# Kernel optimization log

Hardware: AMD Instinct MI355X
Metric: run time of the kernel (lower is better)

## Reference

```python
import jax, jax.numpy as jnp
import numpy as np

B, S, E, H, TB = 2, 2048, 768, 12, 128
D = E // H  # head_dim = 64


def setup_inputs() -> dict:
    key = jax.random.key(0)
    ks = jax.random.split(key, 16)
    def w(k, shape):
        return (jax.random.normal(k, shape, dtype=jnp.float32) * 0.02)
    return {
        "query": jax.random.normal(ks[0], (B, S, E), dtype=jnp.float32),
        "key": jax.random.normal(ks[1], (B, S, E), dtype=jnp.float32),
        "value": jax.random.normal(ks[2], (B, S, E), dtype=jnp.float32),
        "task_bias": jax.random.normal(ks[3], (B, TB), dtype=jnp.float32),
        "attention_mask": jnp.ones((B, S), dtype=jnp.int32),
        # torch.nn.Linear weights are [out, in]
        "Wq": w(ks[4], (E, E)), "bq": jnp.zeros((E,), jnp.float32),
        "Wk": w(ks[5], (E, E)), "bk": jnp.zeros((E,), jnp.float32),
        "Wv": w(ks[6], (E, E)), "bv": jnp.zeros((E,), jnp.float32),
        "Wtb": w(ks[7], (H, TB)), "btb": jnp.zeros((H,), jnp.float32),
        "Wo": w(ks[8], (E, E)), "bo": jnp.zeros((E,), jnp.float32),
    }


def reference(query, key, value, task_bias, attention_mask,
              Wq, bq, Wk, bk, Wv, bv, Wtb, btb, Wo, bo):
    b, s, e = query.shape
    h, d = H, e // H
    # projections (torch Linear: x @ W^T + b), then split heads -> [b, h, s, d]
    q = (query @ Wq.T + bq).reshape(b, s, h, d).transpose(0, 2, 1, 3)
    k = (key @ Wk.T + bk).reshape(b, s, h, d).transpose(0, 2, 1, 3)
    v = (value @ Wv.T + bv).reshape(b, s, h, d).transpose(0, 2, 1, 3)
    # per-head additive task bias: [b, h] -> [b, h, 1, 1]
    tb = (task_bias @ Wtb.T + btb)[:, :, None, None]
    scores = jnp.einsum("bhqd,bhkd->bhqk", q, k) * (1.0 / (d ** 0.5)) + tb
    # 2-D mask broadcasts over query positions: [b, 1, 1, s]
    scores = jnp.where(attention_mask[:, None, None, :] == 0, -jnp.inf, scores)
    attn = jax.nn.softmax(scores, axis=-1)  # dropout is identity in eval mode
    ctx = jnp.einsum("bhqk,bhkd->bhqd", attn, v)
    ctx = ctx.transpose(0, 2, 1, 3).reshape(b, s, e)
    out = ctx @ Wo.T + bo
    return out, attn
```

## Files before the change

kernel.cpp:

```cpp
#include <hip/hip_runtime.h>
#include <math.h>

#define B_  2
#define S_  2048
#define E_  768
#define H_  12
#define TB_ 128
#define D_  64

typedef __attribute__((ext_vector_type(4))) float f32x4;
typedef __attribute__((ext_vector_type(8))) short bf16x8;

__device__ inline unsigned short bf16_rne(float x) {
    unsigned u = __float_as_uint(x);
    unsigned r = u + 0x7FFFu + ((u >> 16) & 1u);
    return (unsigned short)(r >> 16);
}
__device__ inline void split1(float x, unsigned short& h, unsigned short& l) {
    h = bf16_rne(x);
    float hf = __uint_as_float((unsigned)h << 16);
    l = bf16_rne(x - hf);
}

__device__ inline int lds_off(int row, int sh) {
    int ch = sh >> 3;
    int in = sh & 7;
    return row * 64 + (((ch ^ (row & 7)) << 3) | in);
}

__global__ __launch_bounds__(256)
void split_kernel(const float* __restrict__ in, unsigned short* __restrict__ hi,
                  unsigned short* __restrict__ lo, int n4) {
    int i = blockIdx.x * blockDim.x + threadIdx.x;
    int stride = gridDim.x * blockDim.x;
    for (; i < n4; i += stride) {
        float4 v = *(const float4*)&in[(size_t)i * 4];
        ushort4 h, l;
        split1(v.x, h.x, l.x); split1(v.y, h.y, l.y);
        split1(v.z, h.z, l.z); split1(v.w, h.w, l.w);
        *(ushort4*)&hi[(size_t)i * 4] = h;
        *(ushort4*)&lo[(size_t)i * 4] = l;
    }
}

template<int WPRE, int EPI>
__global__ __launch_bounds__(256)
void gemm_mfma(const unsigned short* __restrict__ Ahi_g,
               const unsigned short* __restrict__ Alo_g,
               const unsigned short* __restrict__ Whi_g,
               const unsigned short* __restrict__ Wlo_g,
               const float* __restrict__ Wf_g,
               const float* __restrict__ bias,
               float* __restrict__ Cf,
               unsigned short* __restrict__ Chi, unsigned short* __restrict__ Clo,
               int M, int N, int K) {
    __shared__ unsigned short Ahi[128 * 64];
    __shared__ unsigned short Alo[128 * 64];
    __shared__ unsigned short Whi[128 * 64];
    __shared__ unsigned short Wlo[128 * 64];

    const int m0 = blockIdx.y * 128;
    const int n0 = blockIdx.x * 128;
    const int tid  = threadIdx.x;
    const int wv   = tid >> 6;
    const int lane = tid & 63;
    const int l15  = lane & 15;
    const int quad = lane >> 4;

    f32x4 acc[2][8] = {};

    for (int k0 = 0; k0 < K; k0 += 64) {
        #pragma unroll
        for (int it = 0; it < 4; ++it) {
            int idx = it * 256 + tid;
            int r = idx >> 3, c8 = idx & 7;
            int o = r * 64 + (((c8 ^ (r & 7)) << 3));
            size_t ga = (size_t)(m0 + r) * K + k0 + c8 * 8;
            *(bf16x8*)&Ahi[o] = *(const bf16x8*)&Ahi_g[ga];
            *(bf16x8*)&Alo[o] = *(const bf16x8*)&Alo_g[ga];
            if constexpr (WPRE) {
                size_t gw = (size_t)(n0 + r) * K + k0 + c8 * 8;
                *(bf16x8*)&Whi[o] = *(const bf16x8*)&Whi_g[gw];
                *(bf16x8*)&Wlo[o] = *(const bf16x8*)&Wlo_g[gw];
            }
        }
        if constexpr (!WPRE) {
            const int row = tid >> 4, c4 = tid & 15;
            #pragma unroll
            for (int ps = 0; ps < 8; ++ps) {
                int r = ps * 16 + row;
                float4 w = *(const float4*)&Wf_g[(size_t)(n0 + r) * K + k0 + c4 * 4];
                ushort4 wh, wl;
                split1(w.x, wh.x, wl.x); split1(w.y, wh.y, wl.y);
                split1(w.z, wh.z, wl.z); split1(w.w, wh.w, wl.w);
                int o = lds_off(r, c4 * 4);
                *(ushort4*)&Whi[o] = wh;  *(ushort4*)&Wlo[o] = wl;
            }
        }
        __syncthreads();

        #pragma unroll
        for (int kk = 0; kk < 64; kk += 32) {
            bf16x8 aHi[2], aLo[2];
            #pragma unroll
            for (int ti = 0; ti < 2; ++ti) {
                int ar = wv * 32 + ti * 16 + l15;
                int sh = kk + quad * 8;
                aHi[ti] = *(const bf16x8*)&Ahi[lds_off(ar, sh)];
                aLo[ti] = *(const bf16x8*)&Alo[lds_off(ar, sh)];
            }
            #pragma unroll
            for (int tj = 0; tj < 8; ++tj) {
                int br = tj * 16 + l15;
                int sh = kk + quad * 8;
                bf16x8 bHi = *(const bf16x8*)&Whi[lds_off(br, sh)];
                bf16x8 bLo = *(const bf16x8*)&Wlo[lds_off(br, sh)];
                #pragma unroll
                for (int ti = 0; ti < 2; ++ti) {
                    acc[ti][tj] = __builtin_amdgcn_mfma_f32_16x16x32_bf16(aHi[ti], bHi, acc[ti][tj], 0, 0, 0);
                    acc[ti][tj] = __builtin_amdgcn_mfma_f32_16x16x32_bf16(aHi[ti], bLo, acc[ti][tj], 0, 0, 0);
                    acc[ti][tj] = __builtin_amdgcn_mfma_f32_16x16x32_bf16(aLo[ti], bHi, acc[ti][tj], 0, 0, 0);
                }
            }
        }
        __syncthreads();
    }

    #pragma unroll
    for (int ti = 0; ti < 2; ++ti) {
        const int ib = m0 + wv * 32 + ti * 16 + quad * 4;
        #pragma unroll
        for (int tj = 0; tj < 8; ++tj) {
            int col = n0 + tj * 16 + l15;
            float bv = bias[col];
            f32x4 a = acc[ti][tj];
            #pragma unroll
            for (int r = 0; r < 4; ++r) {
                float val = a[r] + bv;
                if constexpr (EPI == 0) {
                    Cf[(size_t)(ib + r) * N + col] = val;
                } else if constexpr (EPI == 1) {
                    unsigned short hh, ll;
                    split1(val, hh, ll);
                    Chi[(size_t)(ib + r) * N + col] = hh;
                    Clo[(size_t)(ib + r) * N + col] = ll;
                } else {
                    int token = ib + r;
                    int bt = token >> 11, s = token & (S_ - 1);
                    int hh_ = col >> 6, d = col & 63;
                    size_t oa = ((size_t)(bt * H_ + hh_) * 64 + d) * S_ + s;
                    unsigned short hh, ll;
                    split1(val, hh, ll);
                    Chi[oa] = hh;
                    Clo[oa] = ll;
                }
            }
        }
    }
}

__global__ void tb_kernel(const float* __restrict__ task_bias,
                          const float* __restrict__ Wtb,
                          const float* __restrict__ btb,
                          float* __restrict__ tb) {
    int t = threadIdx.x;
    if (t < B_ * H_) {
        int b = t / H_, h = t % H_;
        float s = 0.f;
        for (int i = 0; i < TB_; ++i)
            s += task_bias[b * TB_ + i] * Wtb[h * TB_ + i];
        tb[t] = s + btb[h];
    }
}

__global__ __launch_bounds__(256)
void scores_kernel(const unsigned short* __restrict__ qhi_g,
                   const unsigned short* __restrict__ qlo_g,
                   const unsigned short* __restrict__ khi_g,
                   const unsigned short* __restrict__ klo_g,
                   const int* __restrict__ mask, const float* __restrict__ tb,
                   float* __restrict__ attn, float* __restrict__ rowsum) {
    __shared__ unsigned short Qhi[128 * 64];
    __shared__ unsigned short Qlo[128 * 64];
    __shared__ unsigned short Khi[128 * 64];
    __shared__ unsigned short Klo[128 * 64];

    const int bh = blockIdx.z;
    const int b = bh / H_, h = bh % H_;
    const int i0 = blockIdx.y * 128;
    const int j0 = blockIdx.x * 128;
    const int tid  = threadIdx.x;
    const int wv   = tid >> 6;
    const int lane = tid & 63;
    const int l15  = lane & 15;
    const int quad = lane >> 4;

    #pragma unroll
    for (int it = 0; it < 4; ++it) {
        int idx = it * 256 + tid;
        int r = idx >> 3, c8 = idx & 7;
        int o = r * 64 + (((c8 ^ (r & 7)) << 3));
        size_t gq = ((size_t)b * S_ + i0 + r) * E_ + h * D_ + c8 * 8;
        size_t gk = ((size_t)b * S_ + j0 + r) * E_ + h * D_ + c8 * 8;
        *(bf16x8*)&Qhi[o] = *(const bf16x8*)&qhi_g[gq];
        *(bf16x8*)&Qlo[o] = *(const bf16x8*)&qlo_g[gq];
        *(bf16x8*)&Khi[o] = *(const bf16x8*)&khi_g[gk];
        *(bf16x8*)&Klo[o] = *(const bf16x8*)&klo_g[gk];
    }
    __syncthreads();

    f32x4 acc[2][8] = {};
    #pragma unroll
    for (int kk = 0; kk < 64; kk += 32) {
        bf16x8 aHi[2], aLo[2];
        #pragma unroll
        for (int ti = 0; ti < 2; ++ti) {
            int ar = wv * 32 + ti * 16 + l15;
            int sh = kk + quad * 8;
            aHi[ti] = *(const bf16x8*)&Qhi[lds_off(ar, sh)];
            aLo[ti] = *(const bf16x8*)&Qlo[lds_off(ar, sh)];
        }
        #pragma unroll
        for (int tj = 0; tj < 8; ++tj) {
            int br = tj * 16 + l15;
            int sh = kk + quad * 8;
            bf16x8 bHi = *(const bf16x8*)&Khi[lds_off(br, sh)];
            bf16x8 bLo = *(const bf16x8*)&Klo[lds_off(br, sh)];
            #pragma unroll
            for (int ti = 0; ti < 2; ++ti) {
                acc[ti][tj] = __builtin_amdgcn_mfma_f32_16x16x32_bf16(aHi[ti], bHi, acc[ti][tj], 0, 0, 0);
                acc[ti][tj] = __builtin_amdgcn_mfma_f32_16x16x32_bf16(aHi[ti], bLo, acc[ti][tj], 0, 0, 0);
                acc[ti][tj] = __builtin_amdgcn_mfma_f32_16x16x32_bf16(aLo[ti], bHi, acc[ti][tj], 0, 0, 0);
            }
        }
    }

    const float tbv = tb[bh];
    const int* mrow = mask + b * S_ + j0;
    int m_[8];
    #pragma unroll
    for (int tj = 0; tj < 8; ++tj) m_[tj] = mrow[tj * 16 + l15];

    float* attnbase = attn + (size_t)bh * S_ * S_;
    #pragma unroll
    for (int ti = 0; ti < 2; ++ti) {
        float rs[4] = {0.f, 0.f, 0.f, 0.f};
        const int ib = i0 + wv * 32 + ti * 16 + quad * 4;
        #pragma unroll
        for (int tj = 0; tj < 8; ++tj) {
            f32x4 a = acc[ti][tj];
            #pragma unroll
            for (int r = 0; r < 4; ++r) {
                float sc = a[r] * 0.125f + tbv;
                float p = m_[tj] ? __expf(sc) : 0.f;
                attnbase[(size_t)(ib + r) * S_ + j0 + tj * 16 + l15] = p;
                rs[r] += p;
            }
        }
        #pragma unroll
        for (int off = 1; off < 16; off <<= 1) {
            #pragma unroll
            for (int r = 0; r < 4; ++r)
                rs[r] += __shfl_xor(rs[r], off, 64);
        }
        if (l15 == 0) {
            #pragma unroll
            for (int r = 0; r < 4; ++r)
                atomicAdd(&rowsum[(size_t)bh * S_ + ib + r], rs[r]);
        }
    }
}

__global__ __launch_bounds__(256)
void ctx_mfma(float* __restrict__ attn, const float* __restrict__ rowsum,
              const unsigned short* __restrict__ Vthi_g,
              const unsigned short* __restrict__ Vtlo_g,
              unsigned short* __restrict__ ctxhi, unsigned short* __restrict__ ctxlo) {
    __shared__ unsigned short Phi[64 * 64];
    __shared__ unsigned short Plo[64 * 64];
    __shared__ unsigned short Vhi[64 * 64];
    __shared__ unsigned short Vlo[64 * 64];
    __shared__ float invs[64];

    const int bh = blockIdx.y;
    const int b = bh / H_, h = bh % H_;
    const int i0 = blockIdx.x * 64;
    const int tid  = threadIdx.x;
    const int wv   = tid >> 6;
    const int lane = tid & 63;
    const int l15  = lane & 15;
    const int quad = lane >> 4;

    if (tid < 64)
        invs[tid] = 1.0f / rowsum[(size_t)bh * S_ + i0 + tid];
    __syncthreads();

    f32x4 acc[4] = {};

    for (int kc = 0; kc < S_; kc += 64) {
        #pragma unroll
        for (int it = 0; it < 4; ++it) {
            int idx = it * 256 + tid;
            int row = idx >> 4, c4 = idx & 15;
            size_t pa = ((size_t)bh * S_ + i0 + row) * S_ + kc + c4 * 4;
            float4 p = *(const float4*)&attn[pa];
            float iv = invs[row];
            p.x *= iv; p.y *= iv; p.z *= iv; p.w *= iv;
            *(float4*)&attn[pa] = p;
            ushort4 ph, pl;
            split1(p.x, ph.x, pl.x); split1(p.y, ph.y, pl.y);
            split1(p.z, ph.z, pl.z); split1(p.w, ph.w, pl.w);
            int o = lds_off(row, c4 * 4);
            *(ushort4*)&Phi[o] = ph;  *(ushort4*)&Plo[o] = pl;
        }
        #pragma unroll
        for (int it = 0; it < 2; ++it) {
            int idx = it * 256 + tid;
            int r = idx >> 3, c8 = idx & 7;
            int o = r * 64 + (((c8 ^ (r & 7)) << 3));
            size_t va = ((size_t)bh * 64 + r) * S_ + kc + c8 * 8;
            *(bf16x8*)&Vhi[o] = *(const bf16x8*)&Vthi_g[va];
            *(bf16x8*)&Vlo[o] = *(const bf16x8*)&Vtlo_g[va];
        }
        __syncthreads();

        #pragma unroll
        for (int kk = 0; kk < 64; kk += 32) {
            int sh = kk + quad * 8;
            bf16x8 aH = *(const bf16x8*)&Phi[lds_off(wv * 16 + l15, sh)];
            bf16x8 aL = *(const bf16x8*)&Plo[lds_off(wv * 16 + l15, sh)];
            #pragma unroll
            for (int tj = 0; tj < 4; ++tj) {
                bf16x8 bH = *(const bf16x8*)&Vhi[lds_off(tj * 16 + l15, sh)];
                bf16x8 bL = *(const bf16x8*)&Vlo[lds_off(tj * 16 + l15, sh)];
                acc[tj] = __builtin_amdgcn_mfma_f32_16x16x32_bf16(aH, bH, acc[tj], 0, 0, 0);
                acc[tj] = __builtin_amdgcn_mfma_f32_16x16x32_bf16(aH, bL, acc[tj], 0, 0, 0);
                acc[tj] = __builtin_amdgcn_mfma_f32_16x16x32_bf16(aL, bH, acc[tj], 0, 0, 0);
            }
        }
        __syncthreads();
    }

    const int ib = i0 + wv * 16 + quad * 4;
    #pragma unroll
    for (int tj = 0; tj < 4; ++tj) {
        int d = tj * 16 + l15;
        f32x4 a = acc[tj];
        #pragma unroll
        for (int r = 0; r < 4; ++r) {
            unsigned short hh, ll;
            split1(a[r], hh, ll);
            size_t oa = ((size_t)b * S_ + ib + r) * E_ + h * D_ + d;
            ctxhi[oa] = hh;
            ctxlo[oa] = ll;
        }
    }
}

extern "C" void kernel_launch(void* const* d_in, const int* in_sizes, int n_in,
                              void* d_out, int out_size, void* d_ws, size_t ws_size,
                              hipStream_t stream) {
    const float* query     = (const float*)d_in[0];
    const float* key       = (const float*)d_in[1];
    const float* value     = (const float*)d_in[2];
    const float* task_bias = (const float*)d_in[3];
    const int*   mask      = (const int*)  d_in[4];
    const float* Wq  = (const float*)d_in[5];
    const float* bq  = (const float*)d_in[6];
    const float* Wk  = (const float*)d_in[7];
    const float* bk  = (const float*)d_in[8];
    const float* Wv  = (const float*)d_in[9];
    const float* bv  = (const float*)d_in[10];
    const float* Wtb = (const float*)d_in[11];
    const float* btb = (const float*)d_in[12];
    const float* Wo  = (const float*)d_in[13];
    const float* bo  = (const float*)d_in[14];

    const size_t BSE = (size_t)B_ * S_ * E_;
    const size_t EE  = (size_t)E_ * E_;
    float* out  = (float*)d_out;
    float* attn = (float*)d_out + BSE;

    unsigned short* qhi  = (unsigned short*)d_ws;
    unsigned short* qlo  = qhi  + BSE;
    unsigned short* khi  = qlo  + BSE;
    unsigned short* klo  = khi  + BSE;
    unsigned short* vthi = klo  + BSE;
    unsigned short* vtlo = vthi + BSE;
    unsigned short* chi  = vtlo + BSE;
    unsigned short* clo  = chi  + BSE;
    float* rowsum = (float*)(clo + BSE);
    float* tbws   = rowsum + (size_t)B_ * H_ * S_;

    unsigned short* aqhi = (unsigned short*)attn;
    unsigned short* aqlo = aqhi + BSE;
    unsigned short* akhi = aqlo + BSE;
    unsigned short* aklo = akhi + BSE;
    unsigned short* avhi = aklo + BSE;
    unsigned short* avlo = avhi + BSE;
    unsigned short* wqhi = avlo + BSE;
    unsigned short* wqlo = wqhi + EE;
    unsigned short* wkhi = wqlo + EE;
    unsigned short* wklo = wkhi + EE;
    unsigned short* wvhi = wklo + EE;
    unsigned short* wvlo = wvhi + EE;

    hipMemsetAsync(rowsum, 0, (size_t)B_ * H_ * S_ * sizeof(float), stream);

    const dim3 blk(256);

    split_kernel<<<dim3(2048), blk, 0, stream>>>(query, aqhi, aqlo, (int)(BSE / 4));
    split_kernel<<<dim3(2048), blk, 0, stream>>>(key,   akhi, aklo, (int)(BSE / 4));
    split_kernel<<<dim3(2048), blk, 0, stream>>>(value, avhi, avlo, (int)(BSE / 4));
    split_kernel<<<dim3(576),  blk, 0, stream>>>(Wq, wqhi, wqlo, (int)(EE / 4));
    split_kernel<<<dim3(576),  blk, 0, stream>>>(Wk, wkhi, wklo, (int)(EE / 4));
    split_kernel<<<dim3(576),  blk, 0, stream>>>(Wv, wvhi, wvlo, (int)(EE / 4));
    tb_kernel<<<1, 64, 0, stream>>>(task_bias, Wtb, btb, tbws);

    const dim3 gProj(E_ / 128, (B_ * S_) / 128);
    gemm_mfma<1, 1><<<gProj, blk, 0, stream>>>(aqhi, aqlo, wqhi, wqlo, nullptr,
                                               bq, nullptr, qhi, qlo,
                                               B_ * S_, E_, E_);
    gemm_mfma<1, 1><<<gProj, blk, 0, stream>>>(akhi, aklo, wkhi, wklo, nullptr,
                                               bk, nullptr, khi, klo,
                                               B_ * S_, E_, E_);
    gemm_mfma<1, 2><<<gProj, blk, 0, stream>>>(avhi, avlo, wvhi, wvlo, nullptr,
                                               bv, nullptr, vthi, vtlo,
                                               B_ * S_, E_, E_);

    const dim3 gSc(S_ / 128, S_ / 128, B_ * H_);
    scores_kernel<<<gSc, blk, 0, stream>>>(qhi, qlo, khi, klo, mask, tbws, attn, rowsum);

    const dim3 gCtx(S_ / 64, B_ * H_);
    ctx_mfma<<<gCtx, blk, 0, stream>>>(attn, rowsum, vthi, vtlo, chi, clo);

    gemm_mfma<0, 0><<<gProj, blk, 0, stream>>>(chi, clo, nullptr, nullptr, Wo,
                                               bo, out, nullptr, nullptr,
                                               B_ * S_, E_, E_);
}
```

Measured before the change: 923.1 us.

## Fuse attention into flash-style kernel and recompute normalized probabilities separately

Replaces the scores-then-context pipeline with a fused kernel that computes unnormalized exp scores, feeds them through LDS into the PV MFMA, and tracks row sums, so the large attn matrix no longer has to be re-read and rewritten by the context kernel. A second kernel then recomputes QK^T and writes the normalized attn output using the stored inverse row sums, which drops the atomics and the memset. The three QKV projections are merged into one launch, and Wo is pre-split into bf16 hi/lo buffers so the output GEMM no longer splits it per tile. The cost is computing QK^T twice and skipping max-subtraction in softmax, which relies on the scores being small enough not to overflow exp.

Result: faster. 812.1 us (-12.0%).

```diff
diff --git a/kernel.cpp b/kernel.cpp
--- a/kernel.cpp
+++ b/kernel.cpp
@@ -43,21 +43,31 @@
     }
 }
 
-template<int WPRE, int EPI>
 __global__ __launch_bounds__(256)
-void gemm_mfma(const unsigned short* __restrict__ Ahi_g,
-               const unsigned short* __restrict__ Alo_g,
-               const unsigned short* __restrict__ Whi_g,
-               const unsigned short* __restrict__ Wlo_g,
-               const float* __restrict__ Wf_g,
-               const float* __restrict__ bias,
-               float* __restrict__ Cf,
-               unsigned short* __restrict__ Chi, unsigned short* __restrict__ Clo,
-               int M, int N, int K) {
-    __shared__ unsigned short Ahi[128 * 64];
-    __shared__ unsigned short Alo[128 * 64];
-    __shared__ unsigned short Whi[128 * 64];
-    __shared__ unsigned short Wlo[128 * 64];
+void qkv_gemm(const unsigned short* __restrict__ aqh, const unsigned short* __restrict__ aql,
+              const unsigned short* __restrict__ akh, const unsigned short* __restrict__ akl,
+              const unsigned short* __restrict__ avh, const unsigned short* __restrict__ avl,
+              const unsigned short* __restrict__ wqh, const unsigned short* __restrict__ wql,
+              const unsigned short* __restrict__ wkh, const unsigned short* __restrict__ wkl,
+              const unsigned short* __restrict__ wvh, const unsigned short* __restrict__ wvl,
+              const float* __restrict__ bq, const float* __restrict__ bk,
+              const float* __restrict__ bv,
+              unsigned short* __restrict__ qh, unsigned short* __restrict__ ql,
+              unsigned short* __restrict__ kh, unsigned short* __restrict__ kl,
+              unsigned short* __restrict__ vth, unsigned short* __restrict__ vtl) {
+    __shared__ unsigned short Ahs[128 * 64];
+    __shared__ unsigned short Als[128 * 64];
+    __shared__ unsigned short Whs[128 * 64];
+    __shared__ unsigned short Wls[128 * 64];
+
+    const int z = blockIdx.z;
+    const unsigned short* Ah_g = z == 0 ? aqh : (z == 1 ? akh : avh);
+    const unsigned short* Al_g = z == 0 ? aql : (z == 1 ? akl : avl);
+    const unsigned short* Wh_g = z == 0 ? wqh : (z == 1 ? wkh : wvh);
+    const unsigned short* Wl_g = z == 0 ? wql : (z == 1 ? wkl : wvl);
+    const float* bias = z == 0 ? bq : (z == 1 ? bk : bv);
+    unsigned short* Ch = z == 0 ? qh : (z == 1 ? kh : vth);
+    unsigned short* Cl = z == 0 ? ql : (z == 1 ? kl : vtl);
 
     const int m0 = blockIdx.y * 128;
     const int n0 = blockIdx.x * 128;
@@ -66,6 +76,7 @@
     const int lane = tid & 63;
     const int l15  = lane & 15;
     const int quad = lane >> 4;
+    const int K = E_, N = E_;
 
     f32x4 acc[2][8] = {};
 
@@ -76,26 +87,11 @@
             int r = idx >> 3, c8 = idx & 7;
             int o = r * 64 + (((c8 ^ (r & 7)) << 3));
             size_t ga = (size_t)(m0 + r) * K + k0 + c8 * 8;
-            *(bf16x8*)&Ahi[o] = *(const bf16x8*)&Ahi_g[ga];
-            *(bf16x8*)&Alo[o] = *(const bf16x8*)&Alo_g[ga];
-            if constexpr (WPRE) {
-                size_t gw = (size_t)(n0 + r) * K + k0 + c8 * 8;
-                *(bf16x8*)&Whi[o] = *(const bf16x8*)&Whi_g[gw];
-                *(bf16x8*)&Wlo[o] = *(const bf16x8*)&Wlo_g[gw];
-            }
-        }
-        if constexpr (!WPRE) {
-            const int row = tid >> 4, c4 = tid & 15;
-            #pragma unroll
-            for (int ps = 0; ps < 8; ++ps) {
-                int r = ps * 16 + row;
-                float4 w = *(const float4*)&Wf_g[(size_t)(n0 + r) * K + k0 + c4 * 4];
-                ushort4 wh, wl;
-                split1(w.x, wh.x, wl.x); split1(w.y, wh.y, wl.y);
-                split1(w.z, wh.z, wl.z); split1(w.w, wh.w, wl.w);
-                int o = lds_off(r, c4 * 4);
-                *(ushort4*)&Whi[o] = wh;  *(ushort4*)&Wlo[o] = wl;
-            }
+            *(bf16x8*)&Ahs[o] = *(const bf16x8*)&Ah_g[ga];
+            *(bf16x8*)&Als[o] = *(const bf16x8*)&Al_g[ga];
+            size_t gw = (size_t)(n0 + r) * K + k0 + c8 * 8;
+            *(bf16x8*)&Whs[o] = *(const bf16x8*)&Wh_g[gw];
+            *(bf16x8*)&Wls[o] = *(const bf16x8*)&Wl_g[gw];
         }
         __syncthreads();
 
@@ -106,15 +102,15 @@
             for (int ti = 0; ti < 2; ++ti) {
                 int ar = wv * 32 + ti * 16 + l15;
                 int sh = kk + quad * 8;
-                aHi[ti] = *(const bf16x8*)&Ahi[lds_off(ar, sh)];
-                aLo[ti] = *(const bf16x8*)&Alo[lds_off(ar, sh)];
+                aHi[ti] = *(const bf16x8*)&Ahs[lds_off(ar, sh)];
+                aLo[ti] = *(const bf16x8*)&Als[lds_off(ar, sh)];
             }
             #pragma unroll
             for (int tj = 0; tj < 8; ++tj) {
                 int br = tj * 16 + l15;
                 int sh = kk + quad * 8;
-                bf16x8 bHi = *(const bf16x8*)&Whi[lds_off(br, sh)];
-                bf16x8 bLo = *(const bf16x8*)&Wlo[lds_off(br, sh)];
+                bf16x8 bHi = *(const bf16x8*)&Whs[lds_off(br, sh)];
+                bf16x8 bLo = *(const bf16x8*)&Wls[lds_off(br, sh)];
                 #pragma unroll
                 for (int ti = 0; ti < 2; ++ti) {
                     acc[ti][tj] = __builtin_amdgcn_mfma_f32_16x16x32_bf16(aHi[ti], bHi, acc[ti][tj], 0, 0, 0);
@@ -132,27 +128,22 @@
         #pragma unroll
         for (int tj = 0; tj < 8; ++tj) {
             int col = n0 + tj * 16 + l15;
-            float bv = bias[col];
+            float bvv = bias[col];
             f32x4 a = acc[ti][tj];
             #pragma unroll
             for (int r = 0; r < 4; ++r) {
-                float val = a[r] + bv;
-                if constexpr (EPI == 0) {
-                    Cf[(size_t)(ib + r) * N + col] = val;
-                } else if constexpr (EPI == 1) {
-                    unsigned short hh, ll;
-                    split1(val, hh, ll);
-                    Chi[(size_t)(ib + r) * N + col] = hh;
-                    Clo[(size_t)(ib + r) * N + col] = ll;
+                float val = a[r] + bvv;
+                unsigned short hh, ll;
+                split1(val, hh, ll);
+                if (z < 2) {
+                    size_t oa = (size_t)(ib + r) * N + col;
+                    Ch[oa] = hh; Cl[oa] = ll;
                 } else {
                     int token = ib + r;
                     int bt = token >> 11, s = token & (S_ - 1);
                     int hh_ = col >> 6, d = col & 63;
                     size_t oa = ((size_t)(bt * H_ + hh_) * 64 + d) * S_ + s;
-                    unsigned short hh, ll;
-                    split1(val, hh, ll);
-                    Chi[oa] = hh;
-                    Clo[oa] = ll;
+                    Ch[oa] = hh; Cl[oa] = ll;
                 }
             }
         }
@@ -173,13 +164,168 @@
     }
 }
 
+__global__ __launch_bounds__(256, 2)
+void attn_fused(const unsigned short* __restrict__ qh_g, const unsigned short* __restrict__ ql_g,
+                const unsigned short* __restrict__ kh_g, const unsigned short* __restrict__ kl_g,
+                const unsigned short* __restrict__ vth_g, const unsigned short* __restrict__ vtl_g,
+                const int* __restrict__ mask, const float* __restrict__ tb,
+                unsigned short* __restrict__ ch_g, unsigned short* __restrict__ cl_g,
+                float* __restrict__ rowsuminv) {
+    __shared__ unsigned short Kh[64 * 64];
+    __shared__ unsigned short Kl[64 * 64];
+    __shared__ unsigned short Vh[64 * 64];
+    __shared__ unsigned short Vl[64 * 64];
+    __shared__ unsigned short Ph[128 * 64];
+    __shared__ unsigned short Pl[128 * 64];
+
+    const int bh = blockIdx.y;
+    const int b = bh / H_, h = bh % H_;
+    const int i0 = blockIdx.x * 128;
+    const int tid  = threadIdx.x;
+    const int wv   = tid >> 6;
+    const int lane = tid & 63;
+    const int l15  = lane & 15;
+    const int quad = lane >> 4;
+
+    bf16x8 qH[2][2], qL[2][2];
+    #pragma unroll
+    for (int ti = 0; ti < 2; ++ti) {
+        int ar = i0 + wv * 32 + ti * 16 + l15;
+        #pragma unroll
+        for (int kh2 = 0; kh2 < 2; ++kh2) {
+            size_t ga = ((size_t)b * S_ + ar) * E_ + h * D_ + kh2 * 32 + quad * 8;
+            qH[ti][kh2] = *(const bf16x8*)&qh_g[ga];
+            qL[ti][kh2] = *(const bf16x8*)&ql_g[ga];
+        }
+    }
+
+    const float tbv = tb[bh];
+    float rs[2][4] = {};
+    f32x4 cacc[2][4] = {};
+
+    #pragma unroll 1
+    for (int jt = 0; jt < S_; jt += 64) {
+        #pragma unroll
+        for (int it = 0; it < 2; ++it) {
+            int idx = it * 256 + tid;
+            int r = idx >> 3, c8 = idx & 7;
+            int o = r * 64 + (((c8 ^ (r & 7)) << 3));
+            size_t gk = ((size_t)b * S_ + jt + r) * E_ + h * D_ + c8 * 8;
+            *(bf16x8*)&Kh[o] = *(const bf16x8*)&kh_g[gk];
+            *(bf16x8*)&Kl[o] = *(const bf16x8*)&kl_g[gk];
+            size_t gv = ((size_t)bh * 64 + r) * S_ + jt + c8 * 8;
+            *(bf16x8*)&Vh[o] = *(const bf16x8*)&vth_g[gv];
+            *(bf16x8*)&Vl[o] = *(const bf16x8*)&vtl_g[gv];
+        }
+        __syncthreads();
+
+        f32x4 sacc[2][4] = {};
+        #pragma unroll
+        for (int kk2 = 0; kk2 < 2; ++kk2) {
+            int sh = kk2 * 32 + quad * 8;
+            #pragma unroll
+            for (int tj = 0; tj < 4; ++tj) {
+                bf16x8 bHi = *(const bf16x8*)&Kh[lds_off(tj * 16 + l15, sh)];
+                bf16x8 bLo = *(const bf16x8*)&Kl[lds_off(tj * 16 + l15, sh)];
+                #pragma unroll
+                for (int ti = 0; ti < 2; ++ti) {
+                    sacc[ti][tj] = __builtin_amdgcn_mfma_f32_16x16x32_bf16(qH[ti][kk2], bHi, sacc[ti][tj], 0, 0, 0);
+                    sacc[ti][tj] = __builtin_amdgcn_mfma_f32_16x16x32_bf16(qH[ti][kk2], bLo, sacc[ti][tj], 0, 0, 0);
+                    sacc[ti][tj] = __builtin_amdgcn_mfma_f32_16x16x32_bf16(qL[ti][kk2], bHi, sacc[ti][tj], 0, 0, 0);
+                }
+            }
+        }
+
+        int m_[4];
+        #pragma unroll
+        for (int tj = 0; tj < 4; ++tj) m_[tj] = mask[b * S_ + jt + tj * 16 + l15];
+
+        #pragma unroll
+        for (int ti = 0; ti < 2; ++ti) {
+            #pragma unroll
+            for (int tj = 0; tj < 4; ++tj) {
+                f32x4 a = sacc[ti][tj];
+                #pragma unroll
+                for (int r = 0; r < 4; ++r) {
+                    float p = m_[tj] ? __expf(a[r] * 0.125f + tbv) : 0.f;
+                    rs[ti][r] += p;
+                    int prow = wv * 32 + ti * 16 + quad * 4 + r;
+                    int pcol = tj * 16 + l15;
+                    unsigned short hh, ll;
+                    split1(p, hh, ll);
+                    int off = prow * 64 + ((((pcol >> 3) ^ (prow & 7)) << 3) | (pcol & 7));
+                    Ph[off] = hh; Pl[off] = ll;
+                }
+            }
+        }
+
+        #pragma unroll
+        for (int kk2 = 0; kk2 < 2; ++kk2) {
+            int sh = kk2 * 32 + quad * 8;
+            bf16x8 aHi[2], aLo[2];
+            #pragma unroll
+            for (int ti = 0; ti < 2; ++ti) {
+                int ar = wv * 32 + ti * 16 + l15;
+                aHi[ti] = *(const bf16x8*)&Ph[lds_off(ar, sh)];
+                aLo[ti] = *(const bf16x8*)&Pl[lds_off(ar, sh)];
+            }
+            #pragma unroll
+            for (int td = 0; td < 4; ++td) {
+                bf16x8 bHi = *(const bf16x8*)&Vh[lds_off(td * 16 + l15, sh)];
+                bf16x8 bLo = *(const bf16x8*)&Vl[lds_off(td * 16 + l15, sh)];
+                #pragma unroll
+                for (int ti = 0; ti < 2; ++ti) {
+                    cacc[ti][td] = __builtin_amdgcn_mfma_f32_16x16x32_bf16(aHi[ti], bHi, cacc[ti][td], 0, 0, 0);
+                    cacc[ti][td] = __builtin_amdgcn_mfma_f32_16x16x32_bf16(aHi[ti], bLo, cacc[ti][td], 0, 0, 0);
+                    cacc[ti][td] = __builtin_amdgcn_mfma_f32_16x16x32_bf16(aLo[ti], bHi, cacc[ti][td], 0, 0, 0);
+                }
+            }
+        }
+        __syncthreads();
+    }
+
+    #pragma unroll
+    for (int ti = 0; ti < 2; ++ti)
+        #pragma unroll
+        for (int r = 0; r < 4; ++r)
+            #pragma unroll
+            for (int off = 1; off < 16; off <<= 1)
+                rs[ti][r] += __shfl_xor(rs[ti][r], off, 64);
+
+    #pragma unroll
+    for (int ti = 0; ti < 2; ++ti) {
+        float inv_[4];
+        #pragma unroll
+        for (int r = 0; r < 4; ++r) {
+            inv_[r] = 1.0f / rs[ti][r];
+            if (l15 == 0) {
+                int row = i0 + wv * 32 + ti * 16 + quad * 4 + r;
+                rowsuminv[(size_t)bh * S_ + row] = inv_[r];
+            }
+        }
+        #pragma unroll
+        for (int td = 0; td < 4; ++td) {
+            #pragma unroll
+            for (int r = 0; r < 4; ++r) {
+                float val = cacc[ti][td][r] * inv_[r];
+                unsigned short hh, ll;
+                split1(val, hh, ll);
+                int row = i0 + wv * 32 + ti * 16 + quad * 4 + r;
+                size_t oa = ((size_t)b * S_ + row) * E_ + h * D_ + td * 16 + l15;
+                ch_g[oa] = hh; cl_g[oa] = ll;
+            }
+        }
+    }
+}
+
 __global__ __launch_bounds__(256)
-void scores_kernel(const unsigned short* __restrict__ qhi_g,
-                   const unsigned short* __restrict__ qlo_g,
-                   const unsigned short* __restrict__ khi_g,
-                   const unsigned short* __restrict__ klo_g,
-                   const int* __restrict__ mask, const float* __restrict__ tb,
-                   float* __restrict__ attn, float* __restrict__ rowsum) {
+void attn_write(const unsigned short* __restrict__ qhi_g,
+                const unsigned short* __restrict__ qlo_g,
+                const unsigned short* __restrict__ khi_g,
+                const unsigned short* __restrict__ klo_g,
+                const int* __restrict__ mask, const float* __restrict__ tb,
+                const float* __restrict__ rowsuminv,
+                float* __restrict__ attn) {
     __shared__ unsigned short Qhi[128 * 64];
     __shared__ unsigned short Qlo[128 * 64];
     __shared__ unsigned short Khi[128 * 64];
@@ -244,115 +390,99 @@
     float* attnbase = attn + (size_t)bh * S_ * S_;
     #pragma unroll
     for (int ti = 0; ti < 2; ++ti) {
-        float rs[4] = {0.f, 0.f, 0.f, 0.f};
         const int ib = i0 + wv * 32 + ti * 16 + quad * 4;
+        float inv_[4];
+        #pragma unroll
+        for (int r = 0; r < 4; ++r)
+            inv_[r] = rowsuminv[(size_t)bh * S_ + ib + r];
         #pragma unroll
         for (int tj = 0; tj < 8; ++tj) {
             f32x4 a = acc[ti][tj];
             #pragma unroll
             for (int r = 0; r < 4; ++r) {
                 float sc = a[r] * 0.125f + tbv;
-                float p = m_[tj] ? __expf(sc) : 0.f;
+                float p = m_[tj] ? __expf(sc) * inv_[r] : 0.f;
                 attnbase[(size_t)(ib + r) * S_ + j0 + tj * 16 + l15] = p;
-                rs[r] += p;
-            }
-        }
-        #pragma unroll
-        for (int off = 1; off < 16; off <<= 1) {
-            #pragma unroll
-            for (int r = 0; r < 4; ++r)
-                rs[r] += __shfl_xor(rs[r], off, 64);
-        }
-        if (l15 == 0) {
-            #pragma unroll
-            for (int r = 0; r < 4; ++r)
-                atomicAdd(&rowsum[(size_t)bh * S_ + ib + r], rs[r]);
+            }
         }
     }
 }
 
 __global__ __launch_bounds__(256)
-void ctx_mfma(float* __restrict__ attn, const float* __restrict__ rowsum,
-              const unsigned short* __restrict__ Vthi_g,
-              const unsigned short* __restrict__ Vtlo_g,
-              unsigned short* __restrict__ ctxhi, unsigned short* __restrict__ ctxlo) {
-    __shared__ unsigned short Phi[64 * 64];
-    __shared__ unsigned short Plo[64 * 64];
-    __shared__ unsigned short Vhi[64 * 64];
-    __shared__ unsigned short Vlo[64 * 64];
-    __shared__ float invs[64];
-
-    const int bh = blockIdx.y;
-    const int b = bh / H_, h = bh % H_;
-    const int i0 = blockIdx.x * 64;
+void out_gemm(const unsigned short* __restrict__ Ahi_g,
+              const unsigned short* __restrict__ Alo_g,
+              const unsigned short* __restrict__ Whi_g,
+              const unsigned short* __restrict__ Wlo_g,
+              const float* __restrict__ bias, float* __restrict__ Cf) {
+    __shared__ unsigned short Ahs[128 * 64];
+    __shared__ unsigned short Als[128 * 64];
+    __shared__ unsigned short Whs[128 * 64];
+    __shared__ unsigned short Wls[128 * 64];
+
+    const int m0 = blockIdx.y * 128;
+    const int n0 = blockIdx.x * 128;
     const int tid  = threadIdx.x;
     const int wv   = tid >> 6;
     const int lane = tid & 63;
     const int l15  = lane & 15;
     const int quad = lane >> 4;
-
-    if (tid < 64)
-        invs[tid] = 1.0f / rowsum[(size_t)bh * S_ + i0 + tid];
-    __syncthreads();
-
-    f32x4 acc[4] = {};
-
-    for (int kc = 0; kc < S_; kc += 64) {
+    const int K = E_, N = E_;
+
+    f32x4 acc[2][8] = {};
+
+    for (int k0 = 0; k0 < K; k0 += 64) {
         #pragma unroll
         for (int it = 0; it < 4; ++it) {
-            int idx = it * 256 + tid;
-            int row = idx >> 4, c4 = idx & 15;
-            size_t pa = ((size_t)bh * S_ + i0 + row) * S_ + kc + c4 * 4;
-            float4 p = *(const float4*)&attn[pa];
-            float iv = invs[row];
-            p.x *= iv; p.y *= iv; p.z *= iv; p.w *= iv;
-            *(float4*)&attn[pa] = p;
-            ushort4 ph, pl;
-            split1(p.x, ph.x, pl.x); split1(p.y, ph.y, pl.y);
-            split1(p.z, ph.z, pl.z); split1(p.w, ph.w, pl.w);
-            int o = lds_off(row, c4 * 4);
-            *(ushort4*)&Phi[o] = ph;  *(ushort4*)&Plo[o] = pl;
-        }
-        #pragma unroll
-        for (int it = 0; it < 2; ++it) {
             int idx = it * 256 + tid;
             int r = idx >> 3, c8 = idx & 7;
             int o = r * 64 + (((c8 ^ (r & 7)) << 3));
-            size_t va = ((size_t)bh * 64 + r) * S_ + kc + c8 * 8;
-            *(bf16x8*)&Vhi[o] = *(const bf16x8*)&Vthi_g[va];
-            *(bf16x8*)&Vlo[o] = *(const bf16x8*)&Vtlo_g[va];
+            size_t ga = (size_t)(m0 + r) * K + k0 + c8 * 8;
+            *(bf16x8*)&Ahs[o] = *(const bf16x8*)&Ahi_g[ga];
+            *(bf16x8*)&Als[o] = *(const bf16x8*)&Alo_g[ga];
+            size_t gw = (size_t)(n0 + r) * K + k0 + c8 * 8;
+            *(bf16x8*)&Whs[o] = *(const bf16x8*)&Whi_g[gw];
+            *(bf16x8*)&Wls[o] = *(const bf16x8*)&Wlo_g[gw];
         }
         __syncthreads();
 
         #pragma unroll
         for (int kk = 0; kk < 64; kk += 32) {
-            int sh = kk + quad * 8;
-            bf16x8 aH = *(const bf16x8*)&Phi[lds_off(wv * 16 + l15, sh)];
-            bf16x8 aL = *(const bf16x8*)&Plo[lds_off(wv * 16 + l15, sh)];
-            #pragma unroll
-            for (int tj = 0; tj < 4; ++tj) {
-                bf16x8 bH = *(const bf16x8*)&Vhi[lds_off(tj * 16 + l15, sh)];
-                bf16x8 bL = *(const bf16x8*)&Vlo[lds_off(tj * 16 + l15, sh)];
-                acc[tj] = __builtin_amdgcn_mfma_f32_16x16x32_bf16(aH, bH, acc[tj], 0, 0, 0);
-                acc[tj] = __builtin_amdgcn_mfma_f32_16x16x32_bf16(aH, bL, acc[tj], 0, 0, 0);
-                acc[tj] = __builtin_amdgcn_mfma_f32_16x16x32_bf16(aL, bH, acc[tj], 0, 0, 0);
+            bf16x8 aHi[2], aLo[2];
+            #pragma unroll
+            for (int ti = 0; ti < 2; ++ti) {
+                int ar = wv * 32 + ti * 16 + l15;
+                int sh = kk + quad * 8;
+                aHi[ti] = *(const bf16x8*)&Ahs[lds_off(ar, sh)];
+                aLo[ti] = *(const bf16x8*)&Als[lds_off(ar, sh)];
+            }
+            #pragma unroll
+            for (int tj = 0; tj < 8; ++tj) {
+                int br = tj * 16 + l15;
+                int sh = kk + quad * 8;
+                bf16x8 bHi = *(const bf16x8*)&Whs[lds_off(br, sh)];
+                bf16x8 bLo = *(const bf16x8*)&Wls[lds_off(br, sh)];
+                #pragma unroll
+                for (int ti = 0; ti < 2; ++ti) {
+                    acc[ti][tj] = __builtin_amdgcn_mfma_f32_16x16x32_bf16(aHi[ti], bHi, acc[ti][tj], 0, 0, 0);
+                    acc[ti][tj] = __builtin_amdgcn_mfma_f32_16x16x32_bf16(aHi[ti], bLo, acc[ti][tj], 0, 0, 0);
+                    acc[ti][tj] = __builtin_amdgcn_mfma_f32_16x16x32_bf16(aLo[ti], bHi, acc[ti][tj], 0, 0, 0);
+                }
             }
         }
         __syncthreads();
     }
 
-    const int ib = i0 + wv * 16 + quad * 4;
-    #pragma unroll
-    for (int tj = 0; tj < 4; ++tj) {
-        int d = tj * 16 + l15;
-        f32x4 a = acc[tj];
-        #pragma unroll
-        for (int r = 0; r < 4; ++r) {
-            unsigned short hh, ll;
-            split1(a[r], hh, ll);
-            size_t oa = ((size_t)b * S_ + ib + r) * E_ + h * D_ + d;
-            ctxhi[oa] = hh;
-            ctxlo[oa] = ll;
+    #pragma unroll
+    for (int ti = 0; ti < 2; ++ti) {
+        const int ib = m0 + wv * 32 + ti * 16 + quad * 4;
+        #pragma unroll
+        for (int tj = 0; tj < 8; ++tj) {
+            int col = n0 + tj * 16 + l15;
+            float bvv = bias[col];
+            f32x4 a = acc[ti][tj];
+            #pragma unroll
+            for (int r = 0; r < 4; ++r)
+                Cf[(size_t)(ib + r) * N + col] = a[r] + bvv;
         }
     }
 }
@@ -389,8 +519,8 @@
     unsigned short* vtlo = vthi + BSE;
     unsigned short* chi  = vtlo + BSE;
     unsigned short* clo  = chi  + BSE;
-    float* rowsum = (float*)(clo + BSE);
-    float* tbws   = rowsum + (size_t)B_ * H_ * S_;
+    float* rsinv  = (float*)(clo + BSE);
+    float* tbws   = rsinv + (size_t)B_ * H_ * S_;
 
     unsigned short* aqhi = (unsigned short*)attn;
     unsigned short* aqlo = aqhi + BSE;
@@ -405,7 +535,8 @@
     unsigned short* wvhi = wklo + EE;
     unsigned short* wvlo = wvhi + EE;
 
-    hipMemsetAsync(rowsum, 0, (size_t)B_ * H_ * S_ * sizeof(float), stream);
+    unsigned short* wohi = vthi;
+    unsigned short* wolo = vthi + EE;
 
     const dim3 blk(256);
 
@@ -417,24 +548,21 @@
     split_kernel<<<dim3(576),  blk, 0, stream>>>(Wv, wvhi, wvlo, (int)(EE / 4));
     tb_kernel<<<1, 64, 0, stream>>>(task_bias, Wtb, btb, tbws);
 
-    const dim3 gProj(E_ / 128, (B_ * S_) / 128);
-    gemm_mfma<1, 1><<<gProj, blk, 0, stream>>>(aqhi, aqlo, wqhi, wqlo, nullptr,
-                                               bq, nullptr, qhi, qlo,
-                                               B_ * S_, E_, E_);
-    gemm_mfma<1, 1><<<gProj, blk, 0, stream>>>(akhi, aklo, wkhi, wklo, nullptr,
-                                               bk, nullptr, khi, klo,
-                                               B_ * S_, E_, E_);
-    gemm_mfma<1, 2><<<gProj, blk, 0, stream>>>(avhi, avlo, wvhi, wvlo, nullptr,
-                                               bv, nullptr, vthi, vtlo,
-                                               B_ * S_, E_, E_);
-
-    const dim3 gSc(S_ / 128, S_ / 128, B_ * H_);
-    scores_kernel<<<gSc, blk, 0, stream>>>(qhi, qlo, khi, klo, mask, tbws, attn, rowsum);
-
-    const dim3 gCtx(S_ / 64, B_ * H_);
-    ctx_mfma<<<gCtx, blk, 0, stream>>>(attn, rowsum, vthi, vtlo, chi, clo);
-
-    gemm_mfma<0, 0><<<gProj, blk, 0, stream>>>(chi, clo, nullptr, nullptr, Wo,
-                                               bo, out, nullptr, nullptr,
-                                               B_ * S_, E_, E_);
-}
+    const dim3 gQKV(E_ / 128, (B_ * S_) / 128, 3);
+    qkv_gemm<<<gQKV, blk, 0, stream>>>(aqhi, aqlo, akhi, aklo, avhi, avlo,
+                                       wqhi, wqlo, wkhi, wklo, wvhi, wvlo,
+                                       bq, bk, bv,
+                                       qhi, qlo, khi, klo, vthi, vtlo);
+
+    const dim3 gA(S_ / 128, B_ * H_);
+    attn_fused<<<gA, blk, 0, stream>>>(qhi, qlo, khi, klo, vthi, vtlo,
+                                       mask, tbws, chi, clo, rsinv);
+
+    split_kernel<<<dim3(576), blk, 0, stream>>>(Wo, wohi, wolo, (int)(EE / 4));
+
+    const dim3 gB(S_ / 128, S_ / 128, B_ * H_);
+    attn_write<<<gB, blk, 0, stream>>>(qhi, qlo, khi, klo, mask, tbws, rsinv, attn);
+
+    const dim3 gO(E_ / 128, (B_ * S_) / 128);
+    out_gemm<<<gO, blk, 0, stream>>>(chi, clo, wohi, wolo, bo, out);
+}
```
